# Kernel optimization log

Measured on AMD Instinct MI355X. Metric: run time of the kernel, lower is better.

The kernel has to match this reference:

```python
import jax, jax.numpy as jnp
import numpy as np

VOCAB = 50000
WORD_EMB = 300
N_QNODE = 3
N_KNODE = 3
HID = 512
N_OUT = 300
N_ANS = 32000
N_LAYERS = 3
MIN_NORM = 1e-15
EPS = 1e-7

# ---- Hyperboloid manifold ops (HGCN convention, curvature c, K = 1/c) ----

def proj_tan0(u):
    # zero out the time coordinate
    return u.at[..., :1].set(0.0)

def expmap0(u, c):
    K = 1.0 / c
    sqrtK = jnp.sqrt(K)
    d = u[..., 1:]
    n = jnp.clip(jnp.linalg.norm(d, axis=-1, keepdims=True), MIN_NORM, None)
    theta = n / sqrtK
    return jnp.concatenate([sqrtK * jnp.cosh(theta), sqrtK * jnp.sinh(theta) * d / n], axis=-1)

def logmap0(x, c):
    K = 1.0 / c
    sqrtK = jnp.sqrt(K)
    d = x[..., 1:]
    n = jnp.clip(jnp.linalg.norm(d, axis=-1, keepdims=True), MIN_NORM, None)
    theta = jnp.clip(x[..., :1] / sqrtK, 1.0 + EPS, None)
    rest = sqrtK * jnp.arccosh(theta) * d / n
    return jnp.concatenate([jnp.zeros_like(rest[..., :1]), rest], axis=-1)

def proj(x, c):
    K = 1.0 / c
    d = x[..., 1:]
    first = jnp.sqrt(jnp.clip(K + jnp.sum(d * d, axis=-1, keepdims=True), EPS, None))
    return jnp.concatenate([first, d], axis=-1)

def hyperbolic_emb(x, c):
    return proj(expmap0(proj_tan0(x), c), c)


def setup_inputs() -> dict:
    key = jax.random.key(0)
    ks = jax.random.split(key, 16)
    B, NQ, NK = 256, 30, 100
    inp = {}
    inp['he_ques_id'] = jax.random.randint(ks[0], (B, NQ, N_QNODE), 0, VOCAB)
    inp['he_kg_id'] = jax.random.randint(ks[1], (B, NK, N_KNODE), 0, VOCAB)
    inp['emb_table'] = jax.random.normal(ks[2], (VOCAB, WORD_EMB), jnp.float32)
    inp['q2h_w'] = jax.random.normal(ks[3], (WORD_EMB * N_QNODE, HID), jnp.float32) * 0.01
    inp['q2h_b'] = jnp.zeros((HID,), jnp.float32)
    inp['k2h_w'] = jax.random.normal(ks[4], (WORD_EMB * N_KNODE, HID), jnp.float32) * 0.01
    inp['k2h_b'] = jnp.zeros((HID,), jnp.float32)
    inp['Wk'] = jax.random.normal(ks[5], (N_LAYERS, HID, HID), jnp.float32) * 0.05
    inp['Wq'] = jax.random.normal(ks[6], (N_LAYERS, HID, HID), jnp.float32) * 0.05
    inp['curv'] = jnp.ones((N_LAYERS + 1,), jnp.float32)
    inp['proj1_w'] = jax.random.normal(ks[7], (2 * HID, HID), jnp.float32) * 0.02
    inp['proj1_b'] = jnp.zeros((HID,), jnp.float32)
    inp['proj2_w'] = jax.random.normal(ks[8], (HID, N_OUT), jnp.float32) * 0.02
    inp['proj2_b'] = jnp.zeros((N_OUT,), jnp.float32)
    inp['glove_cands'] = jax.random.normal(ks[9], (N_ANS, N_OUT), jnp.float32)
    return inp


def reference(he_ques_id, he_kg_id, emb_table, q2h_w, q2h_b, k2h_w, k2h_b,
              Wk, Wq, curv, proj1_w, proj1_b, proj2_w, proj2_b, glove_cands):
    B = he_ques_id.shape[0]
    c0 = curv[0]
    cL = curv[N_LAYERS]

    # embedding lookup + flatten hyperedge nodes
    he_q = emb_table[he_ques_id].reshape(B, he_ques_id.shape[1], -1)  # (B,Nq,900)
    he_k = emb_table[he_kg_id].reshape(B, he_kg_id.shape[1], -1)      # (B,Nk,900)
    he_q = jnp.where(jnp.isnan(he_q), 0.0, he_q)
    he_k = jnp.where(jnp.isnan(he_k), 0.0, he_k)

    he_q = he_q @ q2h_w + q2h_b   # (B,Nq,H)
    he_k = he_k @ k2h_w + k2h_b   # (B,Nk,H)

    q = hyperbolic_emb(he_q, c0)  # (B,Nq,H) on hyperboloid
    k = hyperbolic_emb(he_k, c0)  # (B,Nk,H)

    scale = 1.0 / np.sqrt(HID)
    for i in range(N_LAYERS):
        c_in, c_out = curv[i], curv[i + 1]
        kt = proj_tan0(logmap0(k, c_in))
        qt = proj_tan0(logmap0(q, c_in))
        kp = kt @ Wk[i]
        qp = qt @ Wq[i]
        s = jnp.einsum('bkh,bqh->bkq', kp, qp) * scale
        att_k = jnp.einsum('bkq,bqh->bkh', jax.nn.softmax(s, axis=-1), qt) + kt
        att_q = jnp.einsum('bqk,bkh->bqh', jax.nn.softmax(jnp.swapaxes(s, 1, 2), axis=-1), kt) + qt
        k = proj(expmap0(proj_tan0(att_k), c_out), c_out)
        q = proj(expmap0(proj_tan0(att_q), c_out), c_out)

    # mean pool over hyperedges, concat kg||ques
    last_kq = jnp.concatenate([k.mean(axis=1), q.mean(axis=1)], axis=1)  # (B,2H)
    euc = proj_tan0(logmap0(last_kq, cL))
    h = jax.nn.relu(euc @ proj1_w + proj1_b)
    out = h @ proj2_w + proj2_b               # (B,300)
    sim = out @ glove_cands.T                 # (B,32000)
    pred = jax.nn.log_softmax(sim, axis=1)
    return pred
```

## Files before the change

### kernel.cpp

```cpp
#include <hip/hip_runtime.h>
#include <math.h>

#define BATCH 256
#define NQ 30
#define NK 100
#define HID 512
#define WORD 300
#define KIN 900
#define KP 928
#define NANS 32000
#define NOUT 300
#define NOUTP 384
#define NTG 12
#define NLAYERS 3
#define MQT (BATCH * NQ)
#define MKT (BATCH * NK)
#define SCALE 0.044194173824159216f
#define CLDST 136
#define SST 36
#define PQLD 136
#define QTS 256

typedef __attribute__((ext_vector_type(8))) short bf16x8;
typedef __attribute__((ext_vector_type(4))) float f32x4;
typedef unsigned short ushort_t;

__device__ __forceinline__ unsigned short f2bf(float f) {
  unsigned int u = __float_as_uint(f);
  u = (u + 0x7FFF + ((u >> 16) & 1)) >> 16;
  return (unsigned short)u;
}
__device__ __forceinline__ float bf2f(unsigned short s) {
  return __uint_as_float(((unsigned int)s) << 16);
}

typedef const __attribute__((address_space(1))) unsigned int* gas_u32;
typedef __attribute__((address_space(3))) unsigned int* las_u32;
__device__ __forceinline__ void gld_lds16(const void* g, void* l) {
  __builtin_amdgcn_global_load_lds((gas_u32)g, (las_u32)l, 16, 0, 0);
}

__device__ __forceinline__ int xcd_swz_linear() {
  const int nwg = gridDim.x * gridDim.y;
  const int orig = blockIdx.y * gridDim.x + blockIdx.x;
  const int q = nwg >> 3, r = nwg & 7;
  const int xcd = orig & 7, idx = orig >> 3;
  return (xcd < r ? xcd * (q + 1) : r * (q + 1) + (xcd - r) * q) + idx;
}

__device__ __forceinline__ float waveReduceSum(float v) {
#pragma unroll
  for (int o = 32; o > 0; o >>= 1) v += __shfl_xor(v, o);
  return v;
}
__device__ float blockReduceSum512(float v) {
  __shared__ float sm[8];
  int lane = threadIdx.x & 63, w = threadIdx.x >> 6;
  v = waveReduceSum(v);
  if (lane == 0) sm[w] = v;
  __syncthreads();
  float r = 0.f;
#pragma unroll
  for (int i = 0; i < 8; ++i) r += sm[i];
  __syncthreads();
  return r;
}

template <int SWZB, int BIAS, int OUTF32, int OUTBF16, int ZC0, int RELU>
__global__ __launch_bounds__(256) void mfma_gemm2(
    const ushort_t* __restrict__ A1, const ushort_t* __restrict__ Bt1,
    const float* __restrict__ bias1, float* __restrict__ C1,
    ushort_t* __restrict__ Cb1, int M1b,
    const ushort_t* __restrict__ A2, const ushort_t* __restrict__ Bt2,
    const float* __restrict__ bias2, float* __restrict__ C2,
    ushort_t* __restrict__ Cb2,
    size_t zsA, size_t zsB, size_t zsC,
    int N, int K, int nbias) {
  __shared__ __align__(16) ushort_t smem[128 * CLDST];
  const int wg = xcd_swz_linear();
  const int bx = wg % gridDim.x, by = wg / gridDim.x;
  const int z = blockIdx.z;
  const bool sel = (by >= M1b);
  const ushort_t* A = (sel ? A2 : A1) + z * zsA;
  const ushort_t* Bt = (sel ? Bt2 : Bt1) + z * zsB;
  const float* bias = sel ? bias2 : bias1;
  float* C = (sel ? C2 : C1);
  ushort_t* Cb = (sel ? Cb2 : Cb1);
  if (C) C += z * zsC;
  if (Cb) Cb += z * zsC;
  const int row0 = (sel ? (by - M1b) : by) * 128;
  const int col0 = bx * 128;

  const int tid = threadIdx.x;
  const int lane = tid & 63, w = tid >> 6;
  const int wr = w >> 1, wc = w & 1;
  const int s_r = lane & 15, s_kq = lane >> 4;
  const int nt = K / 32;

  const size_t a_src0 = (size_t)(row0 + (w * 2 + 0) * 16 + s_r) * K + s_kq * 8;
  const size_t a_src1 = (size_t)(row0 + (w * 2 + 1) * 16 + s_r) * K + s_kq * 8;
  const size_t b_lin0 = (size_t)(col0 + (w * 2 + 0) * 16 + s_r) * K + s_kq * 8;
  const size_t b_lin1 = (size_t)(col0 + (w * 2 + 1) * 16 + s_r) * K + s_kq * 8;
  const size_t b_swz0 = ((size_t)(col0 >> 7) * nt) * 4096 + (w * 2 + 0) * 512 + lane * 8;
  const size_t b_swz1 = b_swz0 + 512;

  auto stageAB = [&](int t, int bsel) {
    const int k0 = t * 32;
    ushort_t* Ab = smem + bsel * 4096;
    ushort_t* Bb = smem + 8192 + bsel * 4096;
    gld_lds16(A + a_src0 + k0, Ab + (w * 2 + 0) * 512);
    gld_lds16(A + a_src1 + k0, Ab + (w * 2 + 1) * 512);
    if (SWZB) {
      gld_lds16(Bt + b_swz0 + (size_t)t * 4096, Bb + (w * 2 + 0) * 512);
      gld_lds16(Bt + b_swz1 + (size_t)t * 4096, Bb + (w * 2 + 1) * 512);
    } else {
      gld_lds16(Bt + b_lin0 + k0, Bb + (w * 2 + 0) * 512);
      gld_lds16(Bt + b_lin1 + k0, Bb + (w * 2 + 1) * 512);
    }
  };

  f32x4 acc[4][4];
#pragma unroll
  for (int i = 0; i < 4; ++i)
#pragma unroll
    for (int j = 0; j < 4; ++j) acc[i][j] = (f32x4){0.f, 0.f, 0.f, 0.f};

  stageAB(0, 0);
  __syncthreads();
  for (int t = 0; t < nt; ++t) {
    const int cur = t & 1;
    if (t + 1 < nt) stageAB(t + 1, cur ^ 1);
    const ushort_t* Ab = smem + cur * 4096;
    const ushort_t* Bb = smem + 8192 + cur * 4096;
    bf16x8 af[4], bfr[4];
#pragma unroll
    for (int mi = 0; mi < 4; ++mi)
      af[mi] = *(const bf16x8*)(Ab + (wr * 4 + mi) * 512 + lane * 8);
#pragma unroll
    for (int nj = 0; nj < 4; ++nj)
      bfr[nj] = *(const bf16x8*)(Bb + (wc * 4 + nj) * 512 + lane * 8);
#pragma unroll
    for (int mi = 0; mi < 4; ++mi)
#pragma unroll
      for (int nj = 0; nj < 4; ++nj)
        acc[mi][nj] = __builtin_amdgcn_mfma_f32_16x16x32_bf16(
            af[mi], bfr[nj], acc[mi][nj], 0, 0, 0);
    __syncthreads();
  }

  if (OUTBF16) {
#pragma unroll
    for (int nj = 0; nj < 4; ++nj) {
      const int nl = wc * 64 + nj * 16 + (lane & 15);
      const int n = col0 + nl;
      const float bb = BIAS ? ((n < nbias) ? bias[n] : 0.f) : 0.f;
#pragma unroll
      for (int mi = 0; mi < 4; ++mi) {
        f32x4 v = acc[mi][nj];
#pragma unroll
        for (int r = 0; r < 4; ++r) {
          const int ml = wr * 64 + mi * 16 + (lane >> 4) * 4 + r;
          float val = v[r] + bb;
          if (RELU) val = fmaxf(val, 0.f);
          if (ZC0 && n == 0) val = 0.f;
          smem[ml * CLDST + nl] = f2bf(val);
        }
      }
    }
    __syncthreads();
#pragma unroll
    for (int j = 0; j < 8; ++j) {
      const int e = j * 2048 + tid * 8;
      const int ml = e >> 7, nl = e & 127;
      uint4 v = *(const uint4*)(smem + ml * CLDST + nl);
      *(uint4*)(Cb + (size_t)(row0 + ml) * N + col0 + nl) = v;
    }
  }
  if (OUTF32) {
#pragma unroll
    for (int nj = 0; nj < 4; ++nj) {
      const int n = col0 + wc * 64 + nj * 16 + (lane & 15);
      const float bb = BIAS ? ((n < nbias) ? bias[n] : 0.f) : 0.f;
#pragma unroll
      for (int mi = 0; mi < 4; ++mi) {
        f32x4 v = acc[mi][nj];
#pragma unroll
        for (int r = 0; r < 4; ++r) {
          const int m = row0 + wr * 64 + mi * 16 + (lane >> 4) * 4 + r;
          float val = v[r] + bb;
          if (RELU) val = fmaxf(val, 0.f);
          if (ZC0 && n == 0) val = 0.f;
          C[(size_t)m * N + n] = val;
        }
      }
    }
  }
}

__global__ __launch_bounds__(256) void gather_all_k(
    const int* __restrict__ qid, const int* __restrict__ kid,
    const float* __restrict__ emb, ushort_t* __restrict__ gq,
    ushort_t* __restrict__ gk) {
  int m = blockIdx.x;
  const int* ids;
  ushort_t* outp;
  if (m < MQT) {
    ids = qid + m * 3;
    outp = gq + (size_t)m * KP;
  } else {
    m -= MQT;
    ids = kid + m * 3;
    outp = gk + (size_t)m * KP;
  }
  const int t = threadIdx.x;
  if (t >= KP / 4) return;
  const int k = t * 4;
  ushort4 o = make_ushort4(0, 0, 0, 0);
  if (k < KIN) {
    const int node = (k >= 600) ? 2 : ((k >= 300) ? 1 : 0);
    const int off = k - node * 300;
    const int id = ids[node];
    float4 v = *(const float4*)(emb + (size_t)id * 300 + off);
    if (v.x != v.x) v.x = 0.f;
    if (v.y != v.y) v.y = 0.f;
    if (v.z != v.z) v.z = 0.f;
    if (v.w != v.w) v.w = 0.f;
    o = make_ushort4(f2bf(v.x), f2bf(v.y), f2bf(v.z), f2bf(v.w));
  }
  *(ushort4*)(outp + k) = o;
}

__global__ __launch_bounds__(256) void tcast4_k(
    const float* __restrict__ q2h_w, const float* __restrict__ k2h_w,
    const float* __restrict__ p1w, const float* __restrict__ p2w,
    ushort_t* __restrict__ q2h_wt, ushort_t* __restrict__ k2h_wt,
    ushort_t* __restrict__ p1wt, ushort_t* __restrict__ p2wt) {
  const int z = blockIdx.z;
  const float* src;
  ushort_t* dst;
  int R, Cc, Rp, Cp;
  if (z == 0)      { src = q2h_w; dst = q2h_wt; R = KIN;  Cc = HID;  Rp = KP;   Cp = HID; }
  else if (z == 1) { src = k2h_w; dst = k2h_wt; R = KIN;  Cc = HID;  Rp = KP;   Cp = HID; }
  else if (z == 2) { src = p1w; dst = p1wt; R = 1024; Cc = HID;  Rp = 1024; Cp = HID; }
  else             { src = p2w; dst = p2wt; R = HID;  Cc = NOUT; Rp = HID;  Cp = NOUTP; }
  const int r0 = blockIdx.y * 32, c0 = blockIdx.x * 32;
  if (r0 >= Rp || c0 >= Cp) return;
  __shared__ float t[32][33];
  const int tx = threadIdx.x & 31, ty = threadIdx.x >> 5;
#pragma unroll
  for (int i = 0; i < 4; ++i) {
    int r = r0 + ty + i * 8, c = c0 + tx;
    t[ty + i * 8][tx] = (r < R && c < Cc) ? src[(size_t)r * Cc + c] : 0.f;
  }
  __syncthreads();
#pragma unroll
  for (int i = 0; i < 4; ++i) {
    int c = c0 + ty + i * 8, r = r0 + tx;
    if (c < Cp && r < Rp) dst[(size_t)c * Rp + r] = f2bf(t[tx][ty + i * 8]);
  }
}

__global__ __launch_bounds__(256) void gcast_swz_k(
    const float* __restrict__ glove, ushort_t* __restrict__ gs) {
  const int ts = blockIdx.x, gp = blockIdx.y;
  ushort_t* dst = gs + ((size_t)gp * NTG + ts) * 4096;
  for (int g = threadIdx.x; g < 512; g += 256) {
    const int o = g * 8;
    const int chunk = o >> 9, kq = (o >> 7) & 3, rl = (o >> 3) & 15;
    const int row = gp * 128 + chunk * 16 + rl;
    const int kb = ts * 32 + kq * 8;
    ushort_t tmp[8];
    if (kb + 8 <= NOUT) {
      const float* s = glove + (size_t)row * NOUT + kb;
      float2 a0 = *(const float2*)(s + 0);
      float2 a1 = *(const float2*)(s + 2);
      float2 a2 = *(const float2*)(s + 4);
      float2 a3 = *(const float2*)(s + 6);
      tmp[0] = f2bf(a0.x); tmp[1] = f2bf(a0.y);
      tmp[2] = f2bf(a1.x); tmp[3] = f2bf(a1.y);
      tmp[4] = f2bf(a2.x); tmp[5] = f2bf(a2.y);
      tmp[6] = f2bf(a3.x); tmp[7] = f2bf(a3.y);
    } else {
#pragma unroll
      for (int j = 0; j < 8; ++j) {
        const int k = kb + j;
        tmp[j] = (k < NOUT) ? f2bf(glove[(size_t)row * NOUT + k]) : (ushort_t)0;
      }
    }
    *(ushort4*)(dst + o) = make_ushort4(tmp[0], tmp[1], tmp[2], tmp[3]);
    *(ushort4*)(dst + o + 4) = make_ushort4(tmp[4], tmp[5], tmp[6], tmp[7]);
  }
}

__global__ __launch_bounds__(128) void castrows_k(
    const float* __restrict__ Wk, const float* __restrict__ Wq,
    ushort_t* __restrict__ Wkr, ushort_t* __restrict__ Wqr) {
  const int idx = blockIdx.x;
  const int mat = idx >> 9, row = idx & 511;
  const float* src = (mat < 3 ? Wk + (size_t)mat * HID * HID
                              : Wq + (size_t)(mat - 3) * HID * HID) + (size_t)row * HID;
  ushort_t* dst = (mat < 3 ? Wkr + (size_t)mat * HID * HID
                           : Wqr + (size_t)(mat - 3) * HID * HID) + (size_t)row * HID;
  const int k = threadIdx.x * 4;
  float4 v = *(const float4*)(src + k);
  *(ushort4*)(dst + k) = make_ushort4(f2bf(v.x), f2bf(v.y), f2bf(v.z), f2bf(v.w));
}

__global__ __launch_bounds__(512) void att_fused_k(
    const ushort_t* __restrict__ Qp, const ushort_t* __restrict__ Ktc,
    const ushort_t* __restrict__ Qc, ushort_t* __restrict__ Kn,
    ushort_t* __restrict__ Qn) {
  const int b = blockIdx.y;
  const int c0 = blockIdx.x * 256;
  __shared__ __align__(16) float S_lds[112 * SST];
  __shared__ __align__(16) ushort_t Pq[32 * PQLD];
  __shared__ __align__(16) ushort_t qts[NQ * QTS];
  const int tid = threadIdx.x;
  const int w = tid >> 6, lane = tid & 63;
  const ushort_t* ktb = Ktc + (size_t)b * NK * HID;
  const ushort_t* qtg = Qc + (size_t)b * NQ * HID;

  for (int e = tid; e < NQ * 32; e += 512) {
    const int r = e >> 5, c16 = e & 31;
    gld_lds16(qtg + (size_t)r * HID + c0 + c16 * 8, qts + r * QTS + c16 * 8);
  }

  if (w < 7) {
    const int r = lane & 15, kq = lane >> 4;
    const ushort_t* qpb = Qp + (size_t)b * NQ * HID;
    const int rowA = w * 16 + r;
    const int rowA_c = (rowA < NK) ? rowA : (NK - 1);
    const int qr1 = (16 + r) < NQ ? (16 + r) : NQ - 1;
    f32x4 a0 = {0.f, 0.f, 0.f, 0.f}, a1 = {0.f, 0.f, 0.f, 0.f};
    for (int k0 = 0; k0 < HID; k0 += 32) {
      bf16x8 af = *(const bf16x8*)(ktb + (size_t)rowA_c * HID + k0 + kq * 8);
      bf16x8 b0 = *(const bf16x8*)(qpb + (size_t)r * HID + k0 + kq * 8);
      bf16x8 b1 = *(const bf16x8*)(qpb + (size_t)qr1 * HID + k0 + kq * 8);
      a0 = __builtin_amdgcn_mfma_f32_16x16x32_bf16(af, b0, a0, 0, 0, 0);
      a1 = __builtin_amdgcn_mfma_f32_16x16x32_bf16(af, b1, a1, 0, 0, 0);
    }
    const int q0 = lane & 15, mb = (lane >> 4) * 4;
#pragma unroll
    for (int rr = 0; rr < 4; ++rr) {
      const int mA = w * 16 + mb + rr;
      if (mA < NK) {
        S_lds[mA * SST + q0] = a0[rr] * SCALE;
        if (q0 + 16 < NQ) S_lds[mA * SST + q0 + 16] = a1[rr] * SCALE;
      }
    }
  }
  __syncthreads();
  float e2[NQ];
  float inv2 = 0.f;
  const int kr2 = tid - 32;
  const bool do2b = (kr2 >= 0 && kr2 < NK);
  if (tid < NQ) {
    const int q = tid;
    float m = -1e30f;
    for (int kr = 0; kr < NK; ++kr) m = fmaxf(m, S_lds[kr * SST + q]);
    float s = 0.f;
    for (int kr = 0; kr < NK; ++kr) s += expf(S_lds[kr * SST + q] - m);
    float inv = 1.f / s;
    for (int kr = 0; kr < NK; ++kr)
      Pq[q * PQLD + kr] = f2bf(expf(S_lds[kr * SST + q] - m) * inv);
    for (int kr = NK; kr < 128; ++kr) Pq[q * PQLD + kr] = 0;
  } else if (tid < 32) {
    for (int kr = 0; kr < 128; ++kr) Pq[tid * PQLD + kr] = 0;
  } else if (do2b) {
    float m = -1e30f;
#pragma unroll
    for (int q = 0; q < NQ; ++q) m = fmaxf(m, S_lds[kr2 * SST + q]);
    float s = 0.f;
#pragma unroll
    for (int q = 0; q < NQ; ++q) {
      e2[q] = expf(S_lds[kr2 * SST + q] - m);
      s += e2[q];
    }
    inv2 = 1.f / s;
  }
  __syncthreads();
  ushort_t* Pk = (ushort_t*)S_lds;
  if (do2b) {
    ushort_t* prow = Pk + kr2 * 72;
#pragma unroll
    for (int q = 0; q < NQ; ++q) prow[q] = f2bf(e2[q] * inv2);
    prow[30] = 0;
    prow[31] = 0;
  }
  __syncthreads();

  const int cl = lane & 15, g8 = (lane >> 4) * 8;
  if (w < 4) {
    bf16x8 bk[4];
#pragma unroll
    for (int nt = 0; nt < 4; ++nt) {
      const int coll = w * 64 + nt * 16 + cl;
      union { ushort_t u[8]; bf16x8 v; } pb;
#pragma unroll
      for (int j = 0; j < 8; ++j) {
        const int q = g8 + j;
        pb.u[j] = qts[(q < NQ ? q : NQ - 1) * QTS + coll];
      }
      bk[nt] = pb.v;
    }
    ushort_t* kout = Kn + (size_t)b * NK * HID;
#pragma unroll
    for (int mt = 0; mt < 7; ++mt) {
      bf16x8 af = *(const bf16x8*)(Pk + (mt * 16 + cl) * 72 + g8);
      f32x4 ac[4];
#pragma unroll
      for (int nt = 0; nt < 4; ++nt) {
        ac[nt] = (f32x4){0.f, 0.f, 0.f, 0.f};
        ac[nt] = __builtin_amdgcn_mfma_f32_16x16x32_bf16(af, bk[nt], ac[nt], 0, 0, 0);
      }
#pragma unroll
      for (int nt = 0; nt < 4; ++nt) {
        const int col = c0 + w * 64 + nt * 16 + cl;
#pragma unroll
        for (int r = 0; r < 4; ++r) {
          const int row = mt * 16 + (lane >> 4) * 4 + r;
          if (row < NK) {
            float v = ac[nt][r] + bf2f(ktb[(size_t)row * HID + col]);
            kout[(size_t)row * HID + col] = f2bf(v);
          }
        }
      }
    }
  } else {
    const int w4 = w - 4;
    f32x4 aq[2][4];
#pragma unroll
    for (int mt = 0; mt < 2; ++mt)
#pragma unroll
      for (int nt = 0; nt < 4; ++nt) aq[mt][nt] = (f32x4){0.f, 0.f, 0.f, 0.f};
#pragma unroll
    for (int ks = 0; ks < 4; ++ks) {
      bf16x8 bq[4];
#pragma unroll
      for (int nt = 0; nt < 4; ++nt) {
        const int col = c0 + w4 * 64 + nt * 16 + cl;
        union { ushort_t u[8]; bf16x8 v; } pb;
#pragma unroll
        for (int j = 0; j < 8; ++j) {
          const int kr = ks * 32 + g8 + j;
          pb.u[j] = ktb[(size_t)(kr < NK ? kr : NK - 1) * HID + col];
        }
        bq[nt] = pb.v;
      }
#pragma unroll
      for (int mt = 0; mt < 2; ++mt) {
        bf16x8 af = *(const bf16x8*)(Pq + (mt * 16 + cl) * PQLD + ks * 32 + g8);
#pragma unroll
        for (int nt = 0; nt < 4; ++nt)
          aq[mt][nt] = __builtin_amdgcn_mfma_f32_16x16x32_bf16(af, bq[nt], aq[mt][nt], 0, 0, 0);
      }
    }
    ushort_t* qout = Qn + (size_t)b * NQ * HID;
#pragma unroll
    for (int mt = 0; mt < 2; ++mt)
#pragma unroll
      for (int nt = 0; nt < 4; ++nt) {
        const int coll = w4 * 64 + nt * 16 + cl;
        const int col = c0 + coll;
#pragma unroll
        for (int r = 0; r < 4; ++r) {
          const int row = mt * 16 + (lane >> 4) * 4 + r;
          if (row < NQ) {
            float v = aq[mt][nt][r] + bf2f(qts[row * QTS + coll]);
            qout[(size_t)row * HID + col] = f2bf(v);
          }
        }
      }
  }
}

__global__ __launch_bounds__(512) void finale_k(
    const ushort_t* __restrict__ Kb, const ushort_t* __restrict__ Qb,
    ushort_t* __restrict__ lastb, const float* __restrict__ curv) {
  const int b = blockIdx.x, tid = threadIdx.x;
  const int w = tid >> 6, lane = tid & 63;
  const float c = curv[NLAYERS];
  const float Kc = 1.f / c, sqrtK = sqrtf(Kc);
  __shared__ float fsc[NK + NQ];
  __shared__ float fst[NK + NQ];
  const ushort_t* xkp = Kb + (size_t)b * NK * HID;
  const ushort_t* xqp = Qb + (size_t)b * NQ * HID;

  for (int r = w; r < NK + NQ; r += 8) {
    const ushort_t* row =
        (r < NK) ? (xkp + (size_t)r * HID) : (xqp + (size_t)(r - NK) * HID);
    bf16x8 v = *(const bf16x8*)(row + lane * 8);
    float ss = 0.f;
#pragma unroll
    for (int j = 0; j < 8; ++j) {
      float t = bf2f((unsigned short)v[j]);
      ss = fmaf(t, t, ss);
    }
    ss = waveReduceSum(ss);
    if (lane == 0) {
      float n = fmaxf(sqrtf(ss), 1e-15f);
      float f = sqrtK * sinhf(n / sqrtK) / n;
      fsc[r] = f;
      fst[r] = sqrtf(fmaxf(Kc + f * f * ss, 1e-7f));
    }
  }
  __syncthreads();

  float mk, mq;
  if (tid == 0) {
    float sk = 0.f, sq2 = 0.f;
    for (int r = 0; r < NK; ++r) sk += fst[r];
    for (int r = 0; r < NQ; ++r) sq2 += fst[NK + r];
    mk = sk;
    mq = sq2;
  } else {
    float sk = 0.f, sq2 = 0.f;
    for (int r = 0; r < NK; ++r)
      sk = fmaf(fsc[r], bf2f(xkp[(size_t)r * HID + tid]), sk);
    for (int r = 0; r < NQ; ++r)
      sq2 = fmaf(fsc[NK + r], bf2f(xqp[(size_t)r * HID + tid]), sq2);
    mk = sk;
    mq = sq2;
  }
  mk *= (1.f / NK);
  mq *= (1.f / NQ);

  float sq = ((tid == 0) ? 0.f : mk * mk) + mq * mq;
  float ssall = blockReduceSum512(sq);
  __shared__ float x0sh;
  if (tid == 0) x0sh = mk;
  __syncthreads();
  const float x0 = x0sh;
  const float n = fmaxf(sqrtf(ssall), 1e-15f);
  const float theta = fmaxf(x0 / sqrtK, 1.f + 1e-7f);
  const float rr = sqrtK * acoshf(theta) / n;
  ushort_t* ob = lastb + (size_t)b * 1024;
  ob[tid] = (tid == 0) ? (ushort_t)0 : f2bf(rr * mk);
  ob[512 + tid] = f2bf(rr * mq);
}

__global__ __launch_bounds__(512) void logsoftmax_k(float* __restrict__ x) {
  const int b = blockIdx.x, tid = threadIdx.x;
  float4* row = (float4*)(x + (size_t)b * NANS);
  float m = -3.4e38f, s = 0.f;
  for (int i = tid; i < NANS / 4; i += 512) {
    float4 v = row[i];
    float lm = fmaxf(fmaxf(v.x, v.y), fmaxf(v.z, v.w));
    float nm = fmaxf(m, lm);
    s = s * expf(m - nm) + expf(v.x - nm) + expf(v.y - nm) +
        expf(v.z - nm) + expf(v.w - nm);
    m = nm;
  }
#pragma unroll
  for (int o = 32; o > 0; o >>= 1) {
    float mo = __shfl_xor(m, o);
    float so = __shfl_xor(s, o);
    float nm = fmaxf(m, mo);
    s = s * expf(m - nm) + so * expf(mo - nm);
    m = nm;
  }
  __shared__ float smm[8], sms[8];
  const int w = tid >> 6, lane = tid & 63;
  if (lane == 0) { smm[w] = m; sms[w] = s; }
  __syncthreads();
  float gm = smm[0], gs = sms[0];
#pragma unroll
  for (int i = 1; i < 8; ++i) {
    float nm = fmaxf(gm, smm[i]);
    gs = gs * expf(gm - nm) + sms[i] * expf(smm[i] - nm);
    gm = nm;
  }
  const float lse = gm + logf(gs);
  for (int i = tid; i < NANS / 4; i += 512) {
    float4 v = row[i];
    v.x -= lse; v.y -= lse; v.z -= lse; v.w -= lse;
    row[i] = v;
  }
}

extern "C" void kernel_launch(void* const* d_in, const int* in_sizes, int n_in,
                              void* d_out, int out_size, void* d_ws, size_t ws_size,
                              hipStream_t stream) {
  const int* qid = (const int*)d_in[0];
  const int* kid = (const int*)d_in[1];
  const float* emb = (const float*)d_in[2];
  const float* q2h_w = (const float*)d_in[3];
  const float* q2h_b = (const float*)d_in[4];
  const float* k2h_w = (const float*)d_in[5];
  const float* k2h_b = (const float*)d_in[6];
  const float* Wk = (const float*)d_in[7];
  const float* Wq = (const float*)d_in[8];
  const float* curv = (const float*)d_in[9];
  const float* p1w = (const float*)d_in[10];
  const float* p1b = (const float*)d_in[11];
  const float* p2w = (const float*)d_in[12];
  const float* p2b = (const float*)d_in[13];
  const float* glove = (const float*)d_in[14];
  float* out = (float*)d_out;

  ushort_t* u = (ushort_t*)d_ws;
  ushort_t* Ks0 = u;
  ushort_t* Ks1 = Ks0 + (size_t)MKT * HID;
  ushort_t* Qs0 = Ks1 + (size_t)MKT * HID;
  ushort_t* Qs1 = Qs0 + (size_t)MQT * HID;
  ushort_t* Qps = Qs1 + (size_t)MQT * HID;
  ushort_t* gq = Qps + (size_t)MQT * HID;
  ushort_t* gk = gq + (size_t)MQT * KP;
  ushort_t* q2h_wt = gk + (size_t)MKT * KP;
  ushort_t* k2h_wt = q2h_wt + (size_t)HID * KP;
  ushort_t* Wkr = k2h_wt + (size_t)HID * KP;
  ushort_t* Wqr = Wkr + (size_t)NLAYERS * HID * HID;
  ushort_t* Mb = Wqr + (size_t)NLAYERS * HID * HID;
  ushort_t* p1wt = Mb + (size_t)NLAYERS * HID * HID;
  ushort_t* p2wt = p1wt + (size_t)HID * 1024;
  ushort_t* lastb = p2wt + (size_t)NOUTP * HID;
  ushort_t* h1b = lastb + (size_t)BATCH * 1024;
  ushort_t* o2b = h1b + (size_t)BATCH * HID;
  ushort_t* gsw = o2b + (size_t)BATCH * NOUTP;

  gather_all_k<<<MQT + MKT, 256, 0, stream>>>(qid, kid, emb, gq, gk);
  tcast4_k<<<dim3(16, 32, 4), 256, 0, stream>>>(
      q2h_w, k2h_w, p1w, p2w, q2h_wt, k2h_wt, p1wt, p2wt);
  castrows_k<<<6 * HID, 128, 0, stream>>>(Wk, Wq, Wkr, Wqr);
  gcast_swz_k<<<dim3(NTG, 250), 256, 0, stream>>>(glove, gsw);

  mfma_gemm2<0, 0, 0, 1, 0, 0><<<dim3(HID / 128, HID / 128, NLAYERS), 256, 0, stream>>>(
      Wkr, Wqr, nullptr, nullptr, Mb, HID / 128,
      Wkr, Wqr, nullptr, nullptr, Mb,
      (size_t)HID * HID, (size_t)HID * HID, (size_t)HID * HID, HID, HID, HID);

  mfma_gemm2<0, 1, 0, 1, 1, 0><<<dim3(HID / 128, MQT / 128 + MKT / 128), 256, 0, stream>>>(
      gq, q2h_wt, q2h_b, nullptr, Qs0, MQT / 128,
      gk, k2h_wt, k2h_b, nullptr, Ks0, 0, 0, 0, HID, KP, HID);

  ushort_t* Kc = Ks0;
  ushort_t* Kn = Ks1;
  ushort_t* Qc = Qs0;
  ushort_t* Qn = Qs1;
  for (int i = 0; i < NLAYERS; ++i) {
    mfma_gemm2<0, 0, 0, 1, 0, 0><<<dim3(HID / 128, MQT / 128), 256, 0, stream>>>(
        Qc, Mb + (size_t)i * HID * HID, nullptr, nullptr, Qps, MQT / 128,
        Qc, Mb + (size_t)i * HID * HID, nullptr, nullptr, Qps,
        0, 0, 0, HID, HID, HID);
    att_fused_k<<<dim3(2, BATCH), 512, 0, stream>>>(Qps, Kc, Qc, Kn, Qn);
    ushort_t* t1 = Kc; Kc = Kn; Kn = t1;
    ushort_t* t2 = Qc; Qc = Qn; Qn = t2;
  }

  finale_k<<<BATCH, 512, 0, stream>>>(Kc, Qc, lastb, curv);

  mfma_gemm2<0, 1, 0, 1, 0, 1><<<dim3(HID / 128, BATCH / 128), 256, 0, stream>>>(
      lastb, p1wt, p1b, nullptr, h1b, BATCH / 128,
      lastb, p1wt, p1b, nullptr, h1b, 0, 0, 0, HID, 1024, HID);
  mfma_gemm2<0, 1, 0, 1, 0, 0><<<dim3(NOUTP / 128, BATCH / 128), 256, 0, stream>>>(
      h1b, p2wt, p2b, nullptr, o2b, BATCH / 128,
      h1b, p2wt, p2b, nullptr, o2b, 0, 0, 0, NOUTP, HID, NOUT);
  mfma_gemm2<1, 0, 1, 0, 0, 0><<<dim3(NANS / 128, BATCH / 128), 256, 0, stream>>>(
      o2b, gsw, nullptr, out, nullptr, BATCH / 128,
      o2b, gsw, nullptr, out, nullptr, 0, 0, 0, NANS, NOUTP, NANS);
  logsoftmax_k<<<BATCH, 512, 0, stream>>>(out);
}
```

Before: 417.0 us.

## Split fused attention into score-softmax and PV kernels with global P buffers

The fused attention kernel is split in two. The first kernel computes the score matrix and both softmaxes once per batch and writes the probabilities to global scratch. The second kernel runs over 4 column slices of 128 instead of 2 of 256 and stages K and Q tiles in LDS through direct global-to-LDS loads, so the strided global gathers and residual reads now hit LDS. This removes the duplicated score computation across column blocks and raises grid parallelism, at the cost of an extra launch and a global round trip for P.

```diff
diff --git a/kernel.cpp b/kernel.cpp
--- a/kernel.cpp
+++ b/kernel.cpp
@@ -18,8 +18,8 @@
 #define SCALE 0.044194173824159216f
 #define CLDST 136
 #define SST 36
-#define PQLD 136
-#define QTS 256
+#define PKL 40
+#define PQL 136
 
 typedef __attribute__((ext_vector_type(8))) short bf16x8;
 typedef __attribute__((ext_vector_type(4))) float f32x4;
@@ -306,25 +306,14 @@
   *(ushort4*)(dst + k) = make_ushort4(f2bf(v.x), f2bf(v.y), f2bf(v.z), f2bf(v.w));
 }
 
-__global__ __launch_bounds__(512) void att_fused_k(
-    const ushort_t* __restrict__ Qp, const ushort_t* __restrict__ Ktc,
-    const ushort_t* __restrict__ Qc, ushort_t* __restrict__ Kn,
-    ushort_t* __restrict__ Qn) {
-  const int b = blockIdx.y;
-  const int c0 = blockIdx.x * 256;
+__global__ __launch_bounds__(512) void s_softmax_k(
+    const ushort_t* __restrict__ Ktc, const ushort_t* __restrict__ Qp,
+    ushort_t* __restrict__ Pkg, ushort_t* __restrict__ Pqg) {
+  const int b = blockIdx.x;
   __shared__ __align__(16) float S_lds[112 * SST];
-  __shared__ __align__(16) ushort_t Pq[32 * PQLD];
-  __shared__ __align__(16) ushort_t qts[NQ * QTS];
   const int tid = threadIdx.x;
   const int w = tid >> 6, lane = tid & 63;
   const ushort_t* ktb = Ktc + (size_t)b * NK * HID;
-  const ushort_t* qtg = Qc + (size_t)b * NQ * HID;
-
-  for (int e = tid; e < NQ * 32; e += 512) {
-    const int r = e >> 5, c16 = e & 31;
-    gld_lds16(qtg + (size_t)r * HID + c0 + c16 * 8, qts + r * QTS + c16 * 8);
-  }
-
   if (w < 7) {
     const int r = lane & 15, kq = lane >> 4;
     const ushort_t* qpb = Qp + (size_t)b * NQ * HID;
@@ -350,10 +339,6 @@
     }
   }
   __syncthreads();
-  float e2[NQ];
-  float inv2 = 0.f;
-  const int kr2 = tid - 32;
-  const bool do2b = (kr2 >= 0 && kr2 < NK);
   if (tid < NQ) {
     const int q = tid;
     float m = -1e30f;
@@ -361,66 +346,99 @@
     float s = 0.f;
     for (int kr = 0; kr < NK; ++kr) s += expf(S_lds[kr * SST + q] - m);
     float inv = 1.f / s;
+    ushort_t* pq = Pqg + (size_t)b * 4096 + q * 128;
     for (int kr = 0; kr < NK; ++kr)
-      Pq[q * PQLD + kr] = f2bf(expf(S_lds[kr * SST + q] - m) * inv);
-    for (int kr = NK; kr < 128; ++kr) Pq[q * PQLD + kr] = 0;
+      pq[kr] = f2bf(expf(S_lds[kr * SST + q] - m) * inv);
+    for (int kr = NK; kr < 128; ++kr) pq[kr] = 0;
   } else if (tid < 32) {
-    for (int kr = 0; kr < 128; ++kr) Pq[tid * PQLD + kr] = 0;
-  } else if (do2b) {
+    ushort_t* pq = Pqg + (size_t)b * 4096 + tid * 128;
+    for (int kr = 0; kr < 128; ++kr) pq[kr] = 0;
+  } else if (tid < 32 + NK) {
+    const int kr = tid - 32;
     float m = -1e30f;
 #pragma unroll
-    for (int q = 0; q < NQ; ++q) m = fmaxf(m, S_lds[kr2 * SST + q]);
+    for (int q = 0; q < NQ; ++q) m = fmaxf(m, S_lds[kr * SST + q]);
     float s = 0.f;
+    float e[NQ];
 #pragma unroll
     for (int q = 0; q < NQ; ++q) {
-      e2[q] = expf(S_lds[kr2 * SST + q] - m);
-      s += e2[q];
-    }
-    inv2 = 1.f / s;
-  }
-  __syncthreads();
-  ushort_t* Pk = (ushort_t*)S_lds;
-  if (do2b) {
-    ushort_t* prow = Pk + kr2 * 72;
-#pragma unroll
-    for (int q = 0; q < NQ; ++q) prow[q] = f2bf(e2[q] * inv2);
-    prow[30] = 0;
-    prow[31] = 0;
+      e[q] = expf(S_lds[kr * SST + q] - m);
+      s += e[q];
+    }
+    float inv = 1.f / s;
+    ushort_t* pk = Pkg + (size_t)b * 4096 + kr * 32;
+#pragma unroll
+    for (int q = 0; q < NQ; ++q) pk[q] = f2bf(e[q] * inv);
+    pk[30] = 0;
+    pk[31] = 0;
+  } else if (tid < 32 + 128) {
+    const int kr = tid - 32;
+    ushort_t* pk = Pkg + (size_t)b * 4096 + kr * 32;
+    for (int q = 0; q < 32; ++q) pk[q] = 0;
+  }
+}
+
+__global__ __launch_bounds__(512) void pv_k(
+    const ushort_t* __restrict__ Pkg, const ushort_t* __restrict__ Pqg,
+    const ushort_t* __restrict__ Ktc, const ushort_t* __restrict__ Qc,
+    ushort_t* __restrict__ Kn, ushort_t* __restrict__ Qn) {
+  const int b = blockIdx.y;
+  const int c0 = blockIdx.x * 128;
+  __shared__ __align__(16) ushort_t kts[NK * 128];
+  __shared__ __align__(16) ushort_t qts[NQ * 128];
+  __shared__ __align__(16) ushort_t Pk_l[128 * PKL];
+  __shared__ __align__(16) ushort_t Pq_l[32 * PQL];
+  const int tid = threadIdx.x;
+  const int w = tid >> 6, lane = tid & 63;
+  const ushort_t* ktb = Ktc + (size_t)b * NK * HID;
+  const ushort_t* qtb = Qc + (size_t)b * NQ * HID;
+
+  for (int e = tid; e < NK * 16; e += 512)
+    gld_lds16(ktb + (size_t)(e >> 4) * HID + c0 + (e & 15) * 8, kts + e * 8);
+  for (int e = tid; e < NQ * 16; e += 512)
+    gld_lds16(qtb + (size_t)(e >> 4) * HID + c0 + (e & 15) * 8, qts + e * 8);
+  {
+    uint4 v1 = *(const uint4*)(Pkg + (size_t)b * 4096 + tid * 8);
+    *(uint4*)(Pk_l + (tid >> 2) * PKL + (tid & 3) * 8) = v1;
+    uint4 v2 = *(const uint4*)(Pqg + (size_t)b * 4096 + tid * 8);
+    *(uint4*)(Pq_l + (tid >> 4) * PQL + (tid & 15) * 8) = v2;
   }
   __syncthreads();
 
   const int cl = lane & 15, g8 = (lane >> 4) * 8;
   if (w < 4) {
-    bf16x8 bk[4];
-#pragma unroll
-    for (int nt = 0; nt < 4; ++nt) {
-      const int coll = w * 64 + nt * 16 + cl;
+    bf16x8 bk[2];
+#pragma unroll
+    for (int nt = 0; nt < 2; ++nt) {
+      const int coll = w * 32 + nt * 16 + cl;
       union { ushort_t u[8]; bf16x8 v; } pb;
 #pragma unroll
       for (int j = 0; j < 8; ++j) {
-        const int q = g8 + j;
-        pb.u[j] = qts[(q < NQ ? q : NQ - 1) * QTS + coll];
+        int q = g8 + j;
+        q = (q < NQ) ? q : (NQ - 1);
+        pb.u[j] = qts[q * 128 + coll];
       }
       bk[nt] = pb.v;
     }
     ushort_t* kout = Kn + (size_t)b * NK * HID;
 #pragma unroll
     for (int mt = 0; mt < 7; ++mt) {
-      bf16x8 af = *(const bf16x8*)(Pk + (mt * 16 + cl) * 72 + g8);
-      f32x4 ac[4];
-#pragma unroll
-      for (int nt = 0; nt < 4; ++nt) {
+      bf16x8 af = *(const bf16x8*)(Pk_l + (mt * 16 + cl) * PKL + g8);
+      f32x4 ac[2];
+#pragma unroll
+      for (int nt = 0; nt < 2; ++nt) {
         ac[nt] = (f32x4){0.f, 0.f, 0.f, 0.f};
         ac[nt] = __builtin_amdgcn_mfma_f32_16x16x32_bf16(af, bk[nt], ac[nt], 0, 0, 0);
       }
 #pragma unroll
-      for (int nt = 0; nt < 4; ++nt) {
-        const int col = c0 + w * 64 + nt * 16 + cl;
+      for (int nt = 0; nt < 2; ++nt) {
+        const int coll = w * 32 + nt * 16 + cl;
+        const int col = c0 + coll;
 #pragma unroll
         for (int r = 0; r < 4; ++r) {
           const int row = mt * 16 + (lane >> 4) * 4 + r;
           if (row < NK) {
-            float v = ac[nt][r] + bf2f(ktb[(size_t)row * HID + col]);
+            float v = ac[nt][r] + bf2f(kts[row * 128 + coll]);
             kout[(size_t)row * HID + col] = f2bf(v);
           }
         }
@@ -428,30 +446,31 @@
     }
   } else {
     const int w4 = w - 4;
-    f32x4 aq[2][4];
+    f32x4 aq[2][2];
 #pragma unroll
     for (int mt = 0; mt < 2; ++mt)
 #pragma unroll
-      for (int nt = 0; nt < 4; ++nt) aq[mt][nt] = (f32x4){0.f, 0.f, 0.f, 0.f};
+      for (int nt = 0; nt < 2; ++nt) aq[mt][nt] = (f32x4){0.f, 0.f, 0.f, 0.f};
 #pragma unroll
     for (int ks = 0; ks < 4; ++ks) {
-      bf16x8 bq[4];
-#pragma unroll
-      for (int nt = 0; nt < 4; ++nt) {
-        const int col = c0 + w4 * 64 + nt * 16 + cl;
+      bf16x8 bq[2];
+#pragma unroll
+      for (int nt = 0; nt < 2; ++nt) {
+        const int coll = w4 * 32 + nt * 16 + cl;
         union { ushort_t u[8]; bf16x8 v; } pb;
 #pragma unroll
         for (int j = 0; j < 8; ++j) {
-          const int kr = ks * 32 + g8 + j;
-          pb.u[j] = ktb[(size_t)(kr < NK ? kr : NK - 1) * HID + col];
+          int kr = ks * 32 + g8 + j;
+          kr = (kr < NK) ? kr : (NK - 1);
+          pb.u[j] = kts[kr * 128 + coll];
         }
         bq[nt] = pb.v;
       }
 #pragma unroll
       for (int mt = 0; mt < 2; ++mt) {
-        bf16x8 af = *(const bf16x8*)(Pq + (mt * 16 + cl) * PQLD + ks * 32 + g8);
-#pragma unroll
-        for (int nt = 0; nt < 4; ++nt)
+        bf16x8 af = *(const bf16x8*)(Pq_l + (mt * 16 + cl) * PQL + ks * 32 + g8);
+#pragma unroll
+        for (int nt = 0; nt < 2; ++nt)
           aq[mt][nt] = __builtin_amdgcn_mfma_f32_16x16x32_bf16(af, bq[nt], aq[mt][nt], 0, 0, 0);
       }
     }
@@ -459,14 +478,14 @@
 #pragma unroll
     for (int mt = 0; mt < 2; ++mt)
 #pragma unroll
-      for (int nt = 0; nt < 4; ++nt) {
-        const int coll = w4 * 64 + nt * 16 + cl;
+      for (int nt = 0; nt < 2; ++nt) {
+        const int coll = w4 * 32 + nt * 16 + cl;
         const int col = c0 + coll;
 #pragma unroll
         for (int r = 0; r < 4; ++r) {
           const int row = mt * 16 + (lane >> 4) * 4 + r;
           if (row < NQ) {
-            float v = aq[mt][nt][r] + bf2f(qts[row * QTS + coll]);
+            float v = aq[mt][nt][r] + bf2f(qts[row * 128 + coll]);
             qout[(size_t)row * HID + col] = f2bf(v);
           }
         }
@@ -617,6 +636,8 @@
   ushort_t* h1b = lastb + (size_t)BATCH * 1024;
   ushort_t* o2b = h1b + (size_t)BATCH * HID;
   ushort_t* gsw = o2b + (size_t)BATCH * NOUTP;
+  ushort_t* Pkg = gsw + (size_t)250 * NTG * 4096;
+  ushort_t* Pqg = Pkg + (size_t)BATCH * 4096;
 
   gather_all_k<<<MQT + MKT, 256, 0, stream>>>(qid, kid, emb, gq, gk);
   tcast4_k<<<dim3(16, 32, 4), 256, 0, stream>>>(
@@ -642,7 +663,8 @@
         Qc, Mb + (size_t)i * HID * HID, nullptr, nullptr, Qps, MQT / 128,
         Qc, Mb + (size_t)i * HID * HID, nullptr, nullptr, Qps,
         0, 0, 0, HID, HID, HID);
-    att_fused_k<<<dim3(2, BATCH), 512, 0, stream>>>(Qps, Kc, Qc, Kn, Qn);
+    s_softmax_k<<<BATCH, 512, 0, stream>>>(Kc, Qps, Pkg, Pqg);
+    pv_k<<<dim3(4, BATCH), 512, 0, stream>>>(Pkg, Pqg, Kc, Qc, Kn, Qn);
     ushort_t* t1 = Kc; Kc = Kn; Kn = t1;
     ushort_t* t2 = Qc; Qc = Qn; Qn = t2;
   }
```

After: 397.7 us. 1.05x faster.
